# Performance work log

Hardware: AMD Instinct MI355X
Metric: run time of the kernel (lower is better)

Reference implementation:

```python
import jax, jax.numpy as jnp
import numpy as np
import math

B, C, H, W = 32, 256, 56, 56
M = 16            # num_frequency_mixtures
MIX = 4           # sqrt(M)
K = 8             # num_fourier_basis + 1
HID = 16
STRIDE = (1, 1)
EPS = 1e-5


def setup_inputs() -> dict:
    key = jax.random.key(0)
    ks = jax.random.split(key, 8)
    return {
        "x": jax.random.normal(ks[0], (B, C, H, W), jnp.float32),
        "fc1_w": jax.random.normal(ks[1], (HID, C), jnp.float32) * 0.08,
        "fc1_b": jnp.zeros((HID,), jnp.float32),
        "ln_g": jnp.ones((HID,), jnp.float32),
        "ln_b": jnp.zeros((HID,), jnp.float32),
        "fh_w": jax.random.normal(ks[2], (C * M * K, HID), jnp.float32) * 0.08,
        "fh_b": jnp.zeros((C * M * K,), jnp.float32),
        "basis_real": jax.random.normal(ks[3], (K, 56, 32), jnp.float32) * 0.5,
        "basis_imag": jax.random.normal(ks[4], (K, 56, 32), jnp.float32) * 0.5,
        "conv_w": jax.random.normal(ks[5], (C, C), jnp.float32) * (1.0 / math.sqrt(C)),
        "bn_g": jnp.ones((C,), jnp.float32),
        "bn_b": jnp.zeros((C,), jnp.float32),
    }


def reference(x, fc1_w, fc1_b, ln_g, ln_b, fh_w, fh_b,
              basis_real, basis_imag, conv_w, bn_g, bn_b):
    b, c, h, w = x.shape
    # --- FrequencyAttention: GAP -> fc1 -> LN -> ReLU -> fourier_head ---
    ctx = x.mean(axis=(2, 3))                          # (B, C)
    hdn = ctx @ fc1_w.T + fc1_b                        # (B, HID)
    mu = hdn.mean(-1, keepdims=True)
    var = hdn.var(-1, keepdims=True)
    hdn = (hdn - mu) / jnp.sqrt(var + EPS) * ln_g + ln_b
    hdn = jax.nn.relu(hdn)
    att = hdn @ fh_w.T + fh_b                          # (B, C*M*K)

    coeffs = jax.nn.softmax(att.reshape(b, c, M, K), axis=-1)  # (B,C,M,K)

    # --- work-canvas sizes ---
    h_out, w_out = h // STRIDE[0], w // STRIDE[1]
    h_work = math.ceil(h / MIX) * MIX                  # 56
    w_f = w // 2 + 1                                   # 29
    w_f_work = math.ceil(w_f / MIX) * MIX              # 32
    w_work = (w_f_work - 1) * 2 if w_f_work > 1 else 1 # 62

    if (h_work, w_work) != (h, w):
        x_work = jax.image.resize(x, (b, c, h_work, w_work), "bilinear")
    else:
        x_work = x

    x_ft = jnp.fft.rfft2(x_work, s=(h_work, w_work), norm="ortho")  # (B,C,Hw,Wfw) complex
    wf = x_ft.shape[-1]                                # == w_f_work
    ph, pwf = h_work // MIX, wf // MIX                 # 14, 8

    basis = jax.lax.complex(basis_real, basis_imag)    # (K, Hw, Wfw)
    basis_p = basis.reshape(K, MIX, ph, MIX, pwf).transpose(1, 3, 0, 2, 4)
    basis_p = basis_p.reshape(M, K, ph, pwf)           # (M,K,ph,pwf)

    x_ft_p = x_ft.reshape(b, c, MIX, ph, MIX, pwf).transpose(0, 2, 4, 1, 3, 5)
    x_ft_p = x_ft_p.reshape(b, M, c, ph, pwf)          # (B,M,C,ph,pwf)

    coeffs_c = jax.lax.complex(coeffs, jnp.zeros_like(coeffs))
    coeffs_p = coeffs_c.transpose(0, 2, 1, 3)          # (B,M,C,K)

    kernel = jnp.einsum("bmck,mkhw->bmchw", coeffs_p, basis_p)  # (B,M,C,ph,pwf)
    out_ft_p = x_ft_p * kernel

    out_ft = out_ft_p.reshape(b, MIX, MIX, c, ph, pwf).transpose(0, 3, 1, 4, 2, 5)
    out_ft = out_ft.reshape(b, c, h_work, wf)

    s_work = (h_work // STRIDE[0], w_work // STRIDE[1])
    y = jnp.fft.irfft2(out_ft, s=s_work, norm="ortho")  # (B,C,56,62)

    if y.shape[2:] != (h_out, w_out):
        y = jax.image.resize(y, (b, c, h_out, w_out), "bilinear")

    # --- 1x1 conv + BatchNorm (batch statistics, training-mode math) ---
    y = jnp.einsum("bchw,oc->bohw", y, conv_w)
    m = y.mean(axis=(0, 2, 3))
    v = y.var(axis=(0, 2, 3))
    y = (y - m[None, :, None, None]) / jnp.sqrt(v + EPS)[None, :, None, None]
    y = y * bn_g[None, :, None, None] + bn_b[None, :, None, None]
    return y
```

## Files before the change

kernel.cpp:

```cpp
#include <hip/hip_runtime.h>
#include <math.h>

typedef __attribute__((ext_vector_type(4))) float f32x4;
typedef __attribute__((ext_vector_type(8))) short s16x8;
typedef __attribute__((ext_vector_type(4))) short s16x4;
typedef unsigned short ushort_t;

#define MFMA16(a, b, c) __builtin_amdgcn_mfma_f32_16x16x32_bf16((a), (b), (c), 0, 0, 0)

#define WO_CTX    0u
#define WO_HDN    32768u
#define WO_BNSUM  34816u
#define WO_BNSQ   35840u
#define WO_SCALE  36864u
#define WO_SHIFT  37888u
#define WO_COEF   40960u
#define WO_BMT_H  4235264u
#define WO_BMT_L  4243456u
#define WO_FARE_H 4251648u
#define WO_FARE_L 4268032u
#define WO_FAIM_H 4284416u
#define WO_FAIM_L 4300800u
#define WO_FDRE_H 4317184u
#define WO_FDRE_L 4333568u
#define WO_FDIM_H 4349952u
#define WO_FDIM_L 4366336u
#define WO_DTT_H  4382720u
#define WO_DTT_L  4390912u
#define WO_CW_H   4399104u
#define WO_CW_L   4530176u
#define WO_YBF    4661248u

__device__ __forceinline__ ushort_t f2bf(float f) {
  unsigned int u = __builtin_bit_cast(unsigned int, f);
  unsigned int r = (u + 0x7fffu + ((u >> 16) & 1u)) >> 16;
  return (ushort_t)r;
}
__device__ __forceinline__ float bf2f(ushort_t h) {
  unsigned int u = ((unsigned int)h) << 16;
  return __builtin_bit_cast(float, u);
}

__device__ double bmat_val(int w, int vv) {
  const int v = vv & 31;
  const bool isI = vv >= 32;
  double accR = 0.0, accI = 0.0;
  for (int wp = 0; wp < 62; ++wp) {
    const double src = (wp + 0.5) * (56.0 / 62.0) - 0.5;
    const int w0 = (int)floor(src);
    const double f = src - (double)w0;
    const double s0 = (w0 >= 0 && w0 <= 55) ? (1.0 - f) : 0.0;
    const double s1 = (w0 + 1 >= 0 && w0 + 1 <= 55) ? f : 0.0;
    const double ssum = s0 + s1;
    double wgt = 0.0;
    if (w == w0) wgt = s0 / ssum;
    else if (w == w0 + 1) wgt = s1 / ssum;
    if (wgt != 0.0) {
      const int p = (v * wp) % 62;
      const double ang = 6.283185307179586476925286766559 * (double)p / 62.0;
      accR += wgt * cos(ang);
      accI -= wgt * sin(ang);
    }
  }
  const double nrm = 1.0 / sqrt(3472.0);
  return (isI ? accI : accR) * nrm;
}

__device__ double dt_val(int kk, int wq) {
  const int v = (kk < 32) ? kk : kk - 32;
  const bool isI = kk >= 32;
  const double ks = 62.0 / 56.0;
  const double src = (wq + 0.5) * ks - 0.5;
  double wsum = 0.0;
  for (int wp = 0; wp < 62; ++wp) {
    const double xx = fabs(src - (double)wp) / ks;
    if (xx < 1.0) wsum += 1.0 - xx;
  }
  const double cv = (v == 0 || v == 31) ? 1.0 : 2.0;
  double accR = 0.0, accI = 0.0;
  for (int wp = 0; wp < 62; ++wp) {
    const double xx = fabs(src - (double)wp) / ks;
    if (xx >= 1.0) continue;
    const double wgt = (1.0 - xx) / wsum;
    double cc, ss;
    if (v == 0)       { cc = 1.0; ss = 0.0; }
    else if (v == 31) { cc = (wp & 1) ? -1.0 : 1.0; ss = 0.0; }
    else {
      const int p = (v * wp) % 62;
      const double ang = 6.283185307179586476925286766559 * (double)p / 62.0;
      cc = cos(ang); ss = sin(ang);
    }
    accR += wgt * cv * cc;
    accI -= wgt * cv * ss;
  }
  const double nrm = 1.0 / sqrt(3472.0);
  return (isI ? -accI : accR) * nrm;
}

__device__ double dt_val_fixed(int kk, int wq) {
  const int v = (kk < 32) ? kk : kk - 32;
  const bool isI = kk >= 32;
  const double ks = 62.0 / 56.0;
  const double src = (wq + 0.5) * ks - 0.5;
  double wsum = 0.0;
  for (int wp = 0; wp < 62; ++wp) {
    const double xx = fabs(src - (double)wp) / ks;
    if (xx < 1.0) wsum += 1.0 - xx;
  }
  const double cv = (v == 0 || v == 31) ? 1.0 : 2.0;
  double accR = 0.0, accI = 0.0;
  for (int wp = 0; wp < 62; ++wp) {
    const double xx = fabs(src - (double)wp) / ks;
    if (xx >= 1.0) continue;
    const double wgt = (1.0 - xx) / wsum;
    double cc, ss;
    if (v == 0)       { cc = 1.0; ss = 0.0; }
    else if (v == 31) { cc = (wp & 1) ? -1.0 : 1.0; ss = 0.0; }
    else {
      const int p = (v * wp) % 62;
      const double ang = 6.283185307179586476925286766559 * (double)p / 62.0;
      cc = cos(ang); ss = sin(ang);
    }
    accR += wgt * cv * cc;
    accI -= wgt * cv * ss;
  }
  const double nrm = 1.0 / sqrt(3472.0);
  return (isI ? accI : accR) * nrm;
}

__device__ __forceinline__ void emit_hilo(ushort_t* hp, ushort_t* lp, int off, double val) {
  const float fv = (float)val;
  const ushort_t h = f2bf(fv);
  const float hf = bf2f(h);
  const ushort_t l = f2bf((float)(val - (double)hf));
  hp[off] = h;
  lp[off] = l;
}

__global__ void k_const(const float* __restrict__ conv_w,
                        ushort_t* BmT_h, ushort_t* BmT_l,
                        ushort_t* FARe_h, ushort_t* FARe_l,
                        ushort_t* FAIm_h, ushort_t* FAIm_l,
                        ushort_t* FDRe_h, ushort_t* FDRe_l,
                        ushort_t* FDIm_h, ushort_t* FDIm_l,
                        ushort_t* DtT_h, ushort_t* DtT_l,
                        ushort_t* W_h, ushort_t* W_l) {
  const int idx = blockIdx.x * 256 + threadIdx.x;
  if (idx < 4096) {
    const int vv = idx >> 6, k = idx & 63;
    const double v = (k < 56) ? bmat_val(k, vv) : 0.0;
    emit_hilo(BmT_h, BmT_l, idx, v);
  } else if (idx < 36864) {
    const int t = (idx - 4096) & 8191;
    const int which = (idx - 4096) >> 13;
    const int row = t >> 7, k = t & 127;
    double val = 0.0;
    if (row < 56 && k < 112) {
      const int h = (k < 56) ? k : k - 56;
      const double ang = 6.283185307179586476925286766559 *
                         (double)((row * h) % 56) / 56.0;
      const double c = cos(ang), s = sin(ang);
      const bool lowk = (k < 56);
      if (which == 0)      val = lowk ? c : s;
      else if (which == 1) val = lowk ? -s : c;
      else if (which == 2) val = lowk ? c : -s;
      else                 val = lowk ? s : c;
    }
    ushort_t* hp = (which == 0) ? FARe_h : (which == 1) ? FAIm_h : (which == 2) ? FDRe_h : FDIm_h;
    ushort_t* lp = (which == 0) ? FARe_l : (which == 1) ? FAIm_l : (which == 2) ? FDRe_l : FDIm_l;
    emit_hilo(hp, lp, t, val);
  } else if (idx < 40960) {
    const int t = idx - 36864;
    const int w = t >> 6, kk = t & 63;
    const double v = (w < 56) ? dt_val_fixed(kk, w) : 0.0;
    emit_hilo(DtT_h, DtT_l, t, v);
  } else if (idx < 106496) {
    const int t = idx - 40960;
    emit_hilo(W_h, W_l, t, (double)conv_w[t]);
  }
}

__global__ __launch_bounds__(256) void k_gap(const float* __restrict__ x,
                                             float* __restrict__ ctx) {
  const int img = blockIdx.x;
  const int tid = threadIdx.x;
  const float4* p4 = (const float4*)(x + (size_t)img * 3136);
  float s = 0.f;
  for (int i = tid; i < 784; i += 256) {
    const float4 v = p4[i];
    s += v.x + v.y + v.z + v.w;
  }
  for (int off = 32; off > 0; off >>= 1) s += __shfl_down(s, off, 64);
  __shared__ float ls[4];
  if ((tid & 63) == 0) ls[tid >> 6] = s;
  __syncthreads();
  if (tid == 0) ctx[img] = (ls[0] + ls[1] + ls[2] + ls[3]) * (1.0f / 3136.0f);
}

__global__ void k_mlp(const float* __restrict__ ctx, const float* __restrict__ fc1_w,
                      const float* __restrict__ fc1_b, const float* __restrict__ ln_g,
                      const float* __restrict__ ln_b, float* __restrict__ hdn) {
  const int b = blockIdx.x;
  const int j = threadIdx.x;
  __shared__ float h[16];
  if (j < 16) {
    const float* cr = ctx + b * 256;
    const float* wr = fc1_w + j * 256;
    float acc = fc1_b[j];
    for (int c0 = 0; c0 < 256; ++c0) acc = fmaf(cr[c0], wr[c0], acc);
    h[j] = acc;
  }
  __syncthreads();
  if (j < 16) {
    float mu = 0.f, m2 = 0.f;
    for (int t = 0; t < 16; ++t) { mu += h[t]; m2 += h[t] * h[t]; }
    mu *= 0.0625f; m2 *= 0.0625f;
    const float var = m2 - mu * mu;
    const float val = (h[j] - mu) / sqrtf(var + 1e-5f) * ln_g[j] + ln_b[j];
    hdn[b * 16 + j] = fmaxf(val, 0.f);
  }
}

__global__ __launch_bounds__(256) void k_coeffs(const float* __restrict__ hdn,
                                                const float* __restrict__ fh_w,
                                                const float* __restrict__ fh_b,
                                                float* __restrict__ coeffs) {
  const int gid = blockIdx.x * 256 + threadIdx.x;
  const int b = gid >> 12;
  const int cm = gid & 4095;
  float hv[16];
  const float* hp = hdn + b * 16;
#pragma unroll
  for (int j = 0; j < 16; ++j) hv[j] = hp[j];
  const int row0 = cm * 8;
  float a[8];
  float mx = -1e30f;
#pragma unroll
  for (int k = 0; k < 8; ++k) {
    const float* wr = fh_w + (size_t)(row0 + k) * 16;
    float acc = fh_b[row0 + k];
#pragma unroll
    for (int j = 0; j < 16; ++j) acc = fmaf(hv[j], wr[j], acc);
    a[k] = acc;
    mx = fmaxf(mx, acc);
  }
  float s = 0.f;
#pragma unroll
  for (int k = 0; k < 8; ++k) { a[k] = expf(a[k] - mx); s += a[k]; }
  const float inv = 1.f / s;
  float* outp = coeffs + (size_t)gid * 8;
#pragma unroll
  for (int k = 0; k < 8; ++k) outp[k] = a[k] * inv;
}

__global__ __launch_bounds__(256) void k_fft(
    const float* __restrict__ x, const float* __restrict__ coeffs,
    const float* __restrict__ basR, const float* __restrict__ basI,
    const ushort_t* __restrict__ BmT_h, const ushort_t* __restrict__ BmT_l,
    const ushort_t* __restrict__ FARe_h, const ushort_t* __restrict__ FARe_l,
    const ushort_t* __restrict__ FAIm_h, const ushort_t* __restrict__ FAIm_l,
    const ushort_t* __restrict__ FDRe_h, const ushort_t* __restrict__ FDRe_l,
    const ushort_t* __restrict__ FDIm_h, const ushort_t* __restrict__ FDIm_l,
    const ushort_t* __restrict__ DtT_h, const ushort_t* __restrict__ DtT_l,
    ushort_t* __restrict__ ybf) {
  __shared__ __align__(16) ushort_t xa[64 * 72];
  __shared__ __align__(16) ushort_t x1T[32 * 136];
  __shared__ __align__(16) ushort_t x2T[32 * 136];
  __shared__ __align__(16) ushort_t ta[64 * 72];
  __shared__ float gf[3584];
  const int img = blockIdx.x;
  const int tid = threadIdx.x;
  const int wave = tid >> 6, lane = tid & 63, col = lane & 15, quad = lane >> 4;
  const f32x4 zf = {0.f, 0.f, 0.f, 0.f};

  {
    unsigned int* za = (unsigned int*)xa;
    unsigned int* z1 = (unsigned int*)x1T;
    unsigned int* z2 = (unsigned int*)x2T;
    for (int i = tid; i < 2304; i += 256) za[i] = 0u;
    for (int i = tid; i < 2176; i += 256) { z1[i] = 0u; z2[i] = 0u; }
  }
  __syncthreads();

  {
    const float4* xp = (const float4*)(x + (size_t)img * 3136);
    for (int f = tid; f < 784; f += 256) {
      const float4 v = xp[f];
      const int h = f / 14, w4 = (f % 14) * 4;
      s16x4 p;
      p[0] = (short)f2bf(v.x); p[1] = (short)f2bf(v.y);
      p[2] = (short)f2bf(v.z); p[3] = (short)f2bf(v.w);
      *(s16x4*)&xa[h * 72 + w4] = p;
    }
    const float* co = coeffs + (size_t)img * 128;
    for (int q = tid; q < 1792; q += 256) {
      const int u = q >> 5, v = q & 31;
      const int m = (u / 14) * 4 + (v >> 3);
      const float* cm = co + m * 8;
      float gr = 0.f, gi = 0.f;
#pragma unroll
      for (int k = 0; k < 8; ++k) {
        gr = fmaf(cm[k], basR[k * 1792 + q], gr);
        gi = fmaf(cm[k], basI[k * 1792 + q], gi);
      }
      gf[q] = gr;
      gf[1792 + q] = gi;
    }
  }
  __syncthreads();

  {
    const int mt = wave;
    const int arow = (mt * 16 + col) * 72;
    const s16x8 a0 = *(const s16x8*)&xa[arow + quad * 8];
    const s16x8 a1 = *(const s16x8*)&xa[arow + 32 + quad * 8];
    const int h0 = mt * 16 + quad * 4;
    for (int nt = 0; nt < 4; ++nt) {
      const int nrow = nt * 16 + col;
      const s16x8 bh0 = *(const s16x8*)&BmT_h[nrow * 64 + quad * 8];
      const s16x8 bl0 = *(const s16x8*)&BmT_l[nrow * 64 + quad * 8];
      const s16x8 bh1 = *(const s16x8*)&BmT_h[nrow * 64 + 32 + quad * 8];
      const s16x8 bl1 = *(const s16x8*)&BmT_l[nrow * 64 + 32 + quad * 8];
      f32x4 acc = zf;
      acc = MFMA16(a0, bh0, acc);
      acc = MFMA16(a0, bl0, acc);
      acc = MFMA16(a1, bh1, acc);
      acc = MFMA16(a1, bl1, acc);
      if (h0 < 56) {
        s16x4 p;
        p[0] = (short)f2bf(acc[0]); p[1] = (short)f2bf(acc[1]);
        p[2] = (short)f2bf(acc[2]); p[3] = (short)f2bf(acc[3]);
        const int vr = nrow & 31;
        const int kk = (nrow < 32) ? h0 : 56 + h0;
        *(s16x4*)&x1T[vr * 136 + kk] = p;
      }
    }
  }
  __syncthreads();

  {
    const int mt = wave;
    f32x4 accRe[2] = {zf, zf}, accIm[2] = {zf, zf};
    for (int ks = 0; ks < 4; ++ks) {
      const int aoff = (mt * 16 + col) * 128 + ks * 32 + quad * 8;
      const s16x8 aRh = *(const s16x8*)&FARe_h[aoff];
      const s16x8 aRl = *(const s16x8*)&FARe_l[aoff];
      const s16x8 aIh = *(const s16x8*)&FAIm_h[aoff];
      const s16x8 aIl = *(const s16x8*)&FAIm_l[aoff];
#pragma unroll
      for (int nt = 0; nt < 2; ++nt) {
        const s16x8 b = *(const s16x8*)&x1T[(nt * 16 + col) * 136 + ks * 32 + quad * 8];
        accRe[nt] = MFMA16(aRh, b, accRe[nt]);
        accRe[nt] = MFMA16(aRl, b, accRe[nt]);
        accIm[nt] = MFMA16(aIh, b, accIm[nt]);
        accIm[nt] = MFMA16(aIl, b, accIm[nt]);
      }
    }
    const int u0 = mt * 16 + quad * 4;
    if (u0 < 56) {
#pragma unroll
      for (int nt = 0; nt < 2; ++nt) {
        const int v = nt * 16 + col;
        s16x4 pR, pI;
#pragma unroll
        for (int r = 0; r < 4; ++r) {
          const int u = u0 + r;
          const float gr = gf[u * 32 + v];
          const float gi = gf[1792 + u * 32 + v];
          const float re = accRe[nt][r] * gr - accIm[nt][r] * gi;
          const float im = accRe[nt][r] * gi + accIm[nt][r] * gr;
          pR[r] = (short)f2bf(re);
          pI[r] = (short)f2bf(im);
        }
        *(s16x4*)&x2T[v * 136 + u0] = pR;
        *(s16x4*)&x2T[v * 136 + 56 + u0] = pI;
      }
    }
  }
  __syncthreads();

  {
    const int mt = wave;
    f32x4 accRe[2] = {zf, zf}, accIm[2] = {zf, zf};
    for (int ks = 0; ks < 4; ++ks) {
      const int aoff = (mt * 16 + col) * 128 + ks * 32 + quad * 8;
      const s16x8 aRh = *(const s16x8*)&FDRe_h[aoff];
      const s16x8 aRl = *(const s16x8*)&FDRe_l[aoff];
      const s16x8 aIh = *(const s16x8*)&FDIm_h[aoff];
      const s16x8 aIl = *(const s16x8*)&FDIm_l[aoff];
#pragma unroll
      for (int nt = 0; nt < 2; ++nt) {
        const s16x8 b = *(const s16x8*)&x2T[(nt * 16 + col) * 136 + ks * 32 + quad * 8];
        accRe[nt] = MFMA16(aRh, b, accRe[nt]);
        accRe[nt] = MFMA16(aRl, b, accRe[nt]);
        accIm[nt] = MFMA16(aIh, b, accIm[nt]);
        accIm[nt] = MFMA16(aIl, b, accIm[nt]);
      }
    }
    const int h0 = mt * 16 + quad * 4;
#pragma unroll
    for (int nt = 0; nt < 2; ++nt) {
      const int v = nt * 16 + col;
#pragma unroll
      for (int r = 0; r < 4; ++r) {
        ta[(h0 + r) * 72 + v]      = f2bf(accRe[nt][r]);
        ta[(h0 + r) * 72 + 32 + v] = f2bf(accIm[nt][r]);
      }
    }
  }
  __syncthreads();

  {
    const int mt = wave;
    const int arow = (mt * 16 + col) * 72;
    const s16x8 a0 = *(const s16x8*)&ta[arow + quad * 8];
    const s16x8 a1 = *(const s16x8*)&ta[arow + 32 + quad * 8];
    const int h0 = mt * 16 + quad * 4;
    ushort_t* yo = ybf + (size_t)img * 3136;
    for (int nt = 0; nt < 4; ++nt) {
      const int w = nt * 16 + col;
      const s16x8 bh0 = *(const s16x8*)&DtT_h[w * 64 + quad * 8];
      const s16x8 bl0 = *(const s16x8*)&DtT_l[w * 64 + quad * 8];
      const s16x8 bh1 = *(const s16x8*)&DtT_h[w * 64 + 32 + quad * 8];
      const s16x8 bl1 = *(const s16x8*)&DtT_l[w * 64 + 32 + quad * 8];
      f32x4 acc = zf;
      acc = MFMA16(a0, bh0, acc);
      acc = MFMA16(a0, bl0, acc);
      acc = MFMA16(a1, bh1, acc);
      acc = MFMA16(a1, bl1, acc);
      if (h0 < 56 && w < 56) {
#pragma unroll
        for (int r = 0; r < 4; ++r) yo[(h0 + r) * 56 + w] = f2bf(acc[r]);
      }
    }
  }
}

__global__ __launch_bounds__(256) void k_conv(const ushort_t* __restrict__ ybf,
                                              const ushort_t* __restrict__ W_h,
                                              const ushort_t* __restrict__ W_l,
                                              float* __restrict__ z) {
  const int pb = blockIdx.x;
  const int oh = blockIdx.y;
  const int b = blockIdx.z;
  const int tid = threadIdx.x;
  const int wave = tid >> 6, lane = tid & 63, col = lane & 15, quad = lane >> 4;
  const f32x4 zf = {0.f, 0.f, 0.f, 0.f};
  f32x4 acc[8][4];
#pragma unroll
  for (int mt = 0; mt < 8; ++mt)
#pragma unroll
    for (int i = 0; i < 4; ++i) acc[mt][i] = zf;

  const size_t ybase = (size_t)b * 256 * 3136;
  int p0i[4];
  bool act[4];
#pragma unroll
  for (int i = 0; i < 4; ++i) {
    p0i[i] = pb * 256 + (wave * 4 + i) * 16;
    act[i] = p0i[i] < 3136;
  }

  for (int ks = 0; ks < 8; ++ks) {
    const int c0 = ks * 32 + quad * 8;
    s16x8 bfr[4];
#pragma unroll
    for (int i = 0; i < 4; ++i) {
      if (act[i]) {
        s16x8 t;
#pragma unroll
        for (int j = 0; j < 8; ++j)
          t[j] = (short)ybf[ybase + (size_t)(c0 + j) * 3136 + p0i[i] + col];
        bfr[i] = t;
      }
    }
#pragma unroll
    for (int mt = 0; mt < 8; ++mt) {
      const int orow = oh * 128 + mt * 16 + col;
      const s16x8 ah = *(const s16x8*)&W_h[orow * 256 + ks * 32 + quad * 8];
      const s16x8 al = *(const s16x8*)&W_l[orow * 256 + ks * 32 + quad * 8];
#pragma unroll
      for (int i = 0; i < 4; ++i) {
        if (act[i]) {
          acc[mt][i] = MFMA16(ah, bfr[i], acc[mt][i]);
          acc[mt][i] = MFMA16(al, bfr[i], acc[mt][i]);
        }
      }
    }
  }

#pragma unroll
  for (int mt = 0; mt < 8; ++mt) {
#pragma unroll
    for (int i = 0; i < 4; ++i) {
      if (!act[i]) continue;
#pragma unroll
      for (int r = 0; r < 4; ++r) {
        const int o = oh * 128 + mt * 16 + quad * 4 + r;
        z[((size_t)b * 256 + o) * 3136 + p0i[i] + col] = acc[mt][i][r];
      }
    }
  }
}

__global__ __launch_bounds__(256) void k_bnsum(const float* __restrict__ z,
                                               float* __restrict__ bnsum,
                                               float* __restrict__ bnsq) {
  const int bo = blockIdx.x;
  const int tid = threadIdx.x;
  const float4* p4 = (const float4*)(z + (size_t)bo * 3136);
  float s = 0.f, s2 = 0.f;
  for (int i = tid; i < 784; i += 256) {
    const float4 v = p4[i];
    s += v.x + v.y + v.z + v.w;
    s2 += v.x * v.x + v.y * v.y + v.z * v.z + v.w * v.w;
  }
  for (int off = 32; off > 0; off >>= 1) {
    s += __shfl_down(s, off, 64);
    s2 += __shfl_down(s2, off, 64);
  }
  __shared__ float ls[8];
  if ((tid & 63) == 0) { ls[tid >> 6] = s; ls[4 + (tid >> 6)] = s2; }
  __syncthreads();
  if (tid == 0) {
    atomicAdd(bnsum + (bo & 255), ls[0] + ls[1] + ls[2] + ls[3]);
    atomicAdd(bnsq + (bo & 255), ls[4] + ls[5] + ls[6] + ls[7]);
  }
}

__global__ void k_bnstats(const float* __restrict__ bnsum, const float* __restrict__ bnsq,
                          const float* __restrict__ bn_g, const float* __restrict__ bn_b,
                          float* __restrict__ scale, float* __restrict__ shift) {
  const int o = threadIdx.x;
  if (o < 256) {
    const float N = 32.f * 3136.f;
    const float m = bnsum[o] / N;
    const float v = bnsq[o] / N - m * m;
    const float sc = bn_g[o] / sqrtf(v + 1e-5f);
    scale[o] = sc;
    shift[o] = bn_b[o] - m * sc;
  }
}

__global__ __launch_bounds__(256) void k_bnapply(float* __restrict__ z,
                                                 const float* __restrict__ scale,
                                                 const float* __restrict__ shift) {
  const size_t i = ((size_t)blockIdx.x * 256 + threadIdx.x) * 4;
  const int ch = (int)((i / 3136) & 255);
  const float sc = scale[ch], sh = shift[ch];
  float4 v = *(float4*)(z + i);
  v.x = fmaf(v.x, sc, sh);
  v.y = fmaf(v.y, sc, sh);
  v.z = fmaf(v.z, sc, sh);
  v.w = fmaf(v.w, sc, sh);
  *(float4*)(z + i) = v;
}

extern "C" void kernel_launch(void* const* d_in, const int* in_sizes, int n_in,
                              void* d_out, int out_size, void* d_ws, size_t ws_size,
                              hipStream_t stream) {
  const float* x          = (const float*)d_in[0];
  const float* fc1_w      = (const float*)d_in[1];
  const float* fc1_b      = (const float*)d_in[2];
  const float* ln_g       = (const float*)d_in[3];
  const float* ln_b       = (const float*)d_in[4];
  const float* fh_w       = (const float*)d_in[5];
  const float* fh_b       = (const float*)d_in[6];
  const float* basis_real = (const float*)d_in[7];
  const float* basis_imag = (const float*)d_in[8];
  const float* conv_w     = (const float*)d_in[9];
  const float* bn_g       = (const float*)d_in[10];
  const float* bn_b       = (const float*)d_in[11];
  float* out = (float*)d_out;
  char* ws = (char*)d_ws;
  (void)in_sizes; (void)n_in; (void)out_size; (void)ws_size;

  float* ctx   = (float*)(ws + WO_CTX);
  float* hdn   = (float*)(ws + WO_HDN);
  float* bnsum = (float*)(ws + WO_BNSUM);
  float* bnsq  = (float*)(ws + WO_BNSQ);
  float* scale = (float*)(ws + WO_SCALE);
  float* shift = (float*)(ws + WO_SHIFT);
  float* coef  = (float*)(ws + WO_COEF);
  ushort_t* BmT_h  = (ushort_t*)(ws + WO_BMT_H);
  ushort_t* BmT_l  = (ushort_t*)(ws + WO_BMT_L);
  ushort_t* FARe_h = (ushort_t*)(ws + WO_FARE_H);
  ushort_t* FARe_l = (ushort_t*)(ws + WO_FARE_L);
  ushort_t* FAIm_h = (ushort_t*)(ws + WO_FAIM_H);
  ushort_t* FAIm_l = (ushort_t*)(ws + WO_FAIM_L);
  ushort_t* FDRe_h = (ushort_t*)(ws + WO_FDRE_H);
  ushort_t* FDRe_l = (ushort_t*)(ws + WO_FDRE_L);
  ushort_t* FDIm_h = (ushort_t*)(ws + WO_FDIM_H);
  ushort_t* FDIm_l = (ushort_t*)(ws + WO_FDIM_L);
  ushort_t* DtT_h  = (ushort_t*)(ws + WO_DTT_H);
  ushort_t* DtT_l  = (ushort_t*)(ws + WO_DTT_L);
  ushort_t* W_h    = (ushort_t*)(ws + WO_CW_H);
  ushort_t* W_l    = (ushort_t*)(ws + WO_CW_L);
  ushort_t* ybf    = (ushort_t*)(ws + WO_YBF);

  hipMemsetAsync(bnsum, 0, 2048, stream);

  hipLaunchKernelGGL(k_const, dim3(416), dim3(256), 0, stream,
                     conv_w, BmT_h, BmT_l, FARe_h, FARe_l, FAIm_h, FAIm_l,
                     FDRe_h, FDRe_l, FDIm_h, FDIm_l, DtT_h, DtT_l, W_h, W_l);
  hipLaunchKernelGGL(k_gap, dim3(8192), dim3(256), 0, stream, x, ctx);
  hipLaunchKernelGGL(k_mlp, dim3(32), dim3(64), 0, stream,
                     ctx, fc1_w, fc1_b, ln_g, ln_b, hdn);
  hipLaunchKernelGGL(k_coeffs, dim3(512), dim3(256), 0, stream, hdn, fh_w, fh_b, coef);
  hipLaunchKernelGGL(k_fft, dim3(8192), dim3(256), 0, stream,
                     x, coef, basis_real, basis_imag,
                     BmT_h, BmT_l, FARe_h, FARe_l, FAIm_h, FAIm_l,
                     FDRe_h, FDRe_l, FDIm_h, FDIm_l, DtT_h, DtT_l, ybf);
  hipLaunchKernelGGL(k_conv, dim3(13, 2, 32), dim3(256), 0, stream, ybf, W_h, W_l, out);
  hipLaunchKernelGGL(k_bnsum, dim3(8192), dim3(256), 0, stream, out, bnsum, bnsq);
  hipLaunchKernelGGL(k_bnstats, dim3(1), dim3(256), 0, stream,
                     bnsum, bnsq, bn_g, bn_b, scale, shift);
  hipLaunchKernelGGL(k_bnapply, dim3(25088), dim3(256), 0, stream, out, scale, shift);
}
```

Measured before the change: 713.0 us.

## Restructure FFT kernel to one image per wave and fuse BN sums into conv

The FFT kernel now has each wave own one whole image in its own shared-memory slice, with four images per block. This removes the block-wide barriers between FFT stages. The spectral kernel G is built once per block from a pre-interleaved basis stored as packed bf16, and x is loaded straight from global memory into MFMA fragments. The conv kernel stages its activations through shared memory so the loads coalesce, and it accumulates the BatchNorm sums with shuffle reductions and atomics, which removes the separate k_bnsum pass over the output. The trade-offs are more per-wave work and register pressure, and G is now held in lower precision.

```diff
diff --git a/kernel.cpp b/kernel.cpp
--- a/kernel.cpp
+++ b/kernel.cpp
@@ -29,7 +29,8 @@
 #define WO_DTT_L  4390912u
 #define WO_CW_H   4399104u
 #define WO_CW_L   4530176u
-#define WO_YBF    4661248u
+#define WO_BASP   4661248u
+#define WO_YBF    4775936u
 
 __device__ __forceinline__ ushort_t f2bf(float f) {
   unsigned int u = __builtin_bit_cast(unsigned int, f);
@@ -39,6 +40,14 @@
 __device__ __forceinline__ float bf2f(ushort_t h) {
   unsigned int u = ((unsigned int)h) << 16;
   return __builtin_bit_cast(float, u);
+}
+__device__ __forceinline__ s16x8 pack8(float4 a, float4 b) {
+  s16x8 r;
+  r[0] = (short)f2bf(a.x); r[1] = (short)f2bf(a.y);
+  r[2] = (short)f2bf(a.z); r[3] = (short)f2bf(a.w);
+  r[4] = (short)f2bf(b.x); r[5] = (short)f2bf(b.y);
+  r[6] = (short)f2bf(b.z); r[7] = (short)f2bf(b.w);
+  return r;
 }
 
 __device__ double bmat_val(int w, int vv) {
@@ -66,7 +75,7 @@
   return (isI ? accI : accR) * nrm;
 }
 
-__device__ double dt_val(int kk, int wq) {
+__device__ double dt_val_fixed(int kk, int wq) {
   const int v = (kk < 32) ? kk : kk - 32;
   const bool isI = kk >= 32;
   const double ks = 62.0 / 56.0;
@@ -94,37 +103,6 @@
     accI -= wgt * cv * ss;
   }
   const double nrm = 1.0 / sqrt(3472.0);
-  return (isI ? -accI : accR) * nrm;
-}
-
-__device__ double dt_val_fixed(int kk, int wq) {
-  const int v = (kk < 32) ? kk : kk - 32;
-  const bool isI = kk >= 32;
-  const double ks = 62.0 / 56.0;
-  const double src = (wq + 0.5) * ks - 0.5;
-  double wsum = 0.0;
-  for (int wp = 0; wp < 62; ++wp) {
-    const double xx = fabs(src - (double)wp) / ks;
-    if (xx < 1.0) wsum += 1.0 - xx;
-  }
-  const double cv = (v == 0 || v == 31) ? 1.0 : 2.0;
-  double accR = 0.0, accI = 0.0;
-  for (int wp = 0; wp < 62; ++wp) {
-    const double xx = fabs(src - (double)wp) / ks;
-    if (xx >= 1.0) continue;
-    const double wgt = (1.0 - xx) / wsum;
-    double cc, ss;
-    if (v == 0)       { cc = 1.0; ss = 0.0; }
-    else if (v == 31) { cc = (wp & 1) ? -1.0 : 1.0; ss = 0.0; }
-    else {
-      const int p = (v * wp) % 62;
-      const double ang = 6.283185307179586476925286766559 * (double)p / 62.0;
-      cc = cos(ang); ss = sin(ang);
-    }
-    accR += wgt * cv * cc;
-    accI -= wgt * cv * ss;
-  }
-  const double nrm = 1.0 / sqrt(3472.0);
   return (isI ? accI : accR) * nrm;
 }
 
@@ -138,13 +116,15 @@
 }
 
 __global__ void k_const(const float* __restrict__ conv_w,
+                        const float* __restrict__ basR, const float* __restrict__ basI,
                         ushort_t* BmT_h, ushort_t* BmT_l,
                         ushort_t* FARe_h, ushort_t* FARe_l,
                         ushort_t* FAIm_h, ushort_t* FAIm_l,
                         ushort_t* FDRe_h, ushort_t* FDRe_l,
                         ushort_t* FDIm_h, ushort_t* FDIm_l,
                         ushort_t* DtT_h, ushort_t* DtT_l,
-                        ushort_t* W_h, ushort_t* W_l) {
+                        ushort_t* W_h, ushort_t* W_l,
+                        float* basP) {
   const int idx = blockIdx.x * 256 + threadIdx.x;
   if (idx < 4096) {
     const int vv = idx >> 6, k = idx & 63;
@@ -177,6 +157,10 @@
   } else if (idx < 106496) {
     const int t = idx - 40960;
     emit_hilo(W_h, W_l, t, (double)conv_w[t]);
+  } else if (idx < 135168) {
+    const int t = idx - 106496;
+    const int q = t >> 4, r = t & 15, k = r >> 1;
+    basP[t] = (r & 1) ? basI[k * 1792 + q] : basR[k * 1792 + q];
   }
 }
 
@@ -255,7 +239,7 @@
 
 __global__ __launch_bounds__(256) void k_fft(
     const float* __restrict__ x, const float* __restrict__ coeffs,
-    const float* __restrict__ basR, const float* __restrict__ basI,
+    const float* __restrict__ basP,
     const ushort_t* __restrict__ BmT_h, const ushort_t* __restrict__ BmT_l,
     const ushort_t* __restrict__ FARe_h, const ushort_t* __restrict__ FARe_l,
     const ushort_t* __restrict__ FAIm_h, const ushort_t* __restrict__ FAIm_l,
@@ -263,174 +247,208 @@
     const ushort_t* __restrict__ FDIm_h, const ushort_t* __restrict__ FDIm_l,
     const ushort_t* __restrict__ DtT_h, const ushort_t* __restrict__ DtT_l,
     ushort_t* __restrict__ ybf) {
-  __shared__ __align__(16) ushort_t xa[64 * 72];
-  __shared__ __align__(16) ushort_t x1T[32 * 136];
-  __shared__ __align__(16) ushort_t x2T[32 * 136];
-  __shared__ __align__(16) ushort_t ta[64 * 72];
-  __shared__ float gf[3584];
-  const int img = blockIdx.x;
+  __shared__ __align__(16) ushort_t buf[4 * 4600];
+  __shared__ unsigned int Gsh[4 * 1792];
+  const int img0 = blockIdx.x * 4;
   const int tid = threadIdx.x;
   const int wave = tid >> 6, lane = tid & 63, col = lane & 15, quad = lane >> 4;
   const f32x4 zf = {0.f, 0.f, 0.f, 0.f};
+  ushort_t* bufw = buf + wave * 4600;
+  const int img = img0 + wave;
 
   {
-    unsigned int* za = (unsigned int*)xa;
-    unsigned int* z1 = (unsigned int*)x1T;
-    unsigned int* z2 = (unsigned int*)x2T;
-    for (int i = tid; i < 2304; i += 256) za[i] = 0u;
-    for (int i = tid; i < 2176; i += 256) { z1[i] = 0u; z2[i] = 0u; }
+    const int row = lane >> 1, half = lane & 1;
+    s16x8 z8;
+#pragma unroll
+    for (int j = 0; j < 8; ++j) z8[j] = 0;
+    *(s16x8*)&bufw[row * 136 + 112 + half * 8] = z8;
+  }
+
+  for (int it = 0; it < 8; ++it) {
+    if (tid < 224) {
+      const int m = it * 2 + (tid >= 112 ? 1 : 0);
+      const int idx = (tid >= 112) ? tid - 112 : tid;
+      const int u = (m >> 2) * 14 + (idx >> 3);
+      const int v = (m & 3) * 8 + (idx & 7);
+      const int q = u * 32 + v;
+      const float4* bp = (const float4*)(basP + q * 16);
+      const float4 b0 = bp[0], b1 = bp[1], b2 = bp[2], b3 = bp[3];
+#pragma unroll
+      for (int i = 0; i < 4; ++i) {
+        const float* cm = coeffs + ((size_t)(img0 + i) * 16 + m) * 8;
+        float gr = 0.f, gi = 0.f;
+        gr = fmaf(cm[0], b0.x, gr); gi = fmaf(cm[0], b0.y, gi);
+        gr = fmaf(cm[1], b0.z, gr); gi = fmaf(cm[1], b0.w, gi);
+        gr = fmaf(cm[2], b1.x, gr); gi = fmaf(cm[2], b1.y, gi);
+        gr = fmaf(cm[3], b1.z, gr); gi = fmaf(cm[3], b1.w, gi);
+        gr = fmaf(cm[4], b2.x, gr); gi = fmaf(cm[4], b2.y, gi);
+        gr = fmaf(cm[5], b2.z, gr); gi = fmaf(cm[5], b2.w, gi);
+        gr = fmaf(cm[6], b3.x, gr); gi = fmaf(cm[6], b3.y, gi);
+        gr = fmaf(cm[7], b3.z, gr); gi = fmaf(cm[7], b3.w, gi);
+        Gsh[i * 1792 + q] = (((unsigned int)f2bf(gr)) << 16) | (unsigned int)f2bf(gi);
+      }
+    }
   }
   __syncthreads();
 
   {
-    const float4* xp = (const float4*)(x + (size_t)img * 3136);
-    for (int f = tid; f < 784; f += 256) {
-      const float4 v = xp[f];
-      const int h = f / 14, w4 = (f % 14) * 4;
-      s16x4 p;
-      p[0] = (short)f2bf(v.x); p[1] = (short)f2bf(v.y);
-      p[2] = (short)f2bf(v.z); p[3] = (short)f2bf(v.w);
-      *(s16x4*)&xa[h * 72 + w4] = p;
-    }
-    const float* co = coeffs + (size_t)img * 128;
-    for (int q = tid; q < 1792; q += 256) {
-      const int u = q >> 5, v = q & 31;
-      const int m = (u / 14) * 4 + (v >> 3);
-      const float* cm = co + m * 8;
-      float gr = 0.f, gi = 0.f;
-#pragma unroll
-      for (int k = 0; k < 8; ++k) {
-        gr = fmaf(cm[k], basR[k * 1792 + q], gr);
-        gi = fmaf(cm[k], basI[k * 1792 + q], gi);
-      }
-      gf[q] = gr;
-      gf[1792 + q] = gi;
-    }
-  }
-  __syncthreads();
+    const float* xim = x + (size_t)img * 3136;
+#pragma unroll
+    for (int mt = 0; mt < 4; ++mt) {
+      const int h = mt * 16 + col;
+      const int hc = (h < 56) ? h : 55;
+      const float* xr = xim + hc * 56;
+      const float4 xa0 = *(const float4*)(xr + quad * 8);
+      const float4 xa1 = *(const float4*)(xr + quad * 8 + 4);
+      const s16x8 a0 = pack8(xa0, xa1);
+      s16x8 a1;
+      if (quad < 3) {
+        const float4 xb0 = *(const float4*)(xr + 32 + quad * 8);
+        const float4 xb1 = *(const float4*)(xr + 36 + quad * 8);
+        a1 = pack8(xb0, xb1);
+      } else {
+#pragma unroll
+        for (int j = 0; j < 8; ++j) a1[j] = 0;
+      }
+      const int h0 = mt * 16 + quad * 4;
+#pragma unroll
+      for (int nt = 0; nt < 4; ++nt) {
+        const int nrow = nt * 16 + col;
+        const s16x8 bh0 = *(const s16x8*)&BmT_h[nrow * 64 + quad * 8];
+        const s16x8 bl0 = *(const s16x8*)&BmT_l[nrow * 64 + quad * 8];
+        const s16x8 bh1 = *(const s16x8*)&BmT_h[nrow * 64 + 32 + quad * 8];
+        const s16x8 bl1 = *(const s16x8*)&BmT_l[nrow * 64 + 32 + quad * 8];
+        f32x4 acc = zf;
+        acc = MFMA16(a0, bh0, acc);
+        acc = MFMA16(a0, bl0, acc);
+        acc = MFMA16(a1, bh1, acc);
+        acc = MFMA16(a1, bl1, acc);
+        if (h0 < 56) {
+          s16x4 p;
+          p[0] = (short)f2bf(acc[0]); p[1] = (short)f2bf(acc[1]);
+          p[2] = (short)f2bf(acc[2]); p[3] = (short)f2bf(acc[3]);
+          const int vr = nrow & 31;
+          const int kk = (nrow < 32) ? h0 : 56 + h0;
+          *(s16x4*)&bufw[vr * 136 + kk] = p;
+        }
+      }
+    }
+  }
 
   {
-    const int mt = wave;
-    const int arow = (mt * 16 + col) * 72;
-    const s16x8 a0 = *(const s16x8*)&xa[arow + quad * 8];
-    const s16x8 a1 = *(const s16x8*)&xa[arow + 32 + quad * 8];
-    const int h0 = mt * 16 + quad * 4;
-    for (int nt = 0; nt < 4; ++nt) {
-      const int nrow = nt * 16 + col;
-      const s16x8 bh0 = *(const s16x8*)&BmT_h[nrow * 64 + quad * 8];
-      const s16x8 bl0 = *(const s16x8*)&BmT_l[nrow * 64 + quad * 8];
-      const s16x8 bh1 = *(const s16x8*)&BmT_h[nrow * 64 + 32 + quad * 8];
-      const s16x8 bl1 = *(const s16x8*)&BmT_l[nrow * 64 + 32 + quad * 8];
-      f32x4 acc = zf;
-      acc = MFMA16(a0, bh0, acc);
-      acc = MFMA16(a0, bl0, acc);
-      acc = MFMA16(a1, bh1, acc);
-      acc = MFMA16(a1, bl1, acc);
+    s16x8 bf[2][4];
+#pragma unroll
+    for (int nt = 0; nt < 2; ++nt)
+#pragma unroll
+      for (int ks = 0; ks < 4; ++ks)
+        bf[nt][ks] = *(const s16x8*)&bufw[(nt * 16 + col) * 136 + ks * 32 + quad * 8];
+
+#pragma unroll
+    for (int mt = 0; mt < 4; ++mt) {
+      f32x4 aR[2] = {zf, zf}, aI[2] = {zf, zf};
+#pragma unroll
+      for (int ks = 0; ks < 4; ++ks) {
+        const int off = (mt * 16 + col) * 128 + ks * 32 + quad * 8;
+        const s16x8 rh = *(const s16x8*)&FARe_h[off];
+        const s16x8 rl = *(const s16x8*)&FARe_l[off];
+        const s16x8 ih = *(const s16x8*)&FAIm_h[off];
+        const s16x8 il = *(const s16x8*)&FAIm_l[off];
+#pragma unroll
+        for (int nt = 0; nt < 2; ++nt) {
+          aR[nt] = MFMA16(rh, bf[nt][ks], aR[nt]);
+          aR[nt] = MFMA16(rl, bf[nt][ks], aR[nt]);
+          aI[nt] = MFMA16(ih, bf[nt][ks], aI[nt]);
+          aI[nt] = MFMA16(il, bf[nt][ks], aI[nt]);
+        }
+      }
+      const int u0 = mt * 16 + quad * 4;
+      if (u0 < 56) {
+#pragma unroll
+        for (int nt = 0; nt < 2; ++nt) {
+          const int v = nt * 16 + col;
+          s16x4 pR, pI;
+#pragma unroll
+          for (int r = 0; r < 4; ++r) {
+            const unsigned int gp = Gsh[wave * 1792 + (u0 + r) * 32 + v];
+            const float gr = __builtin_bit_cast(float, gp & 0xffff0000u);
+            const float gi = __builtin_bit_cast(float, gp << 16);
+            const float re = aR[nt][r] * gr - aI[nt][r] * gi;
+            const float im = aR[nt][r] * gi + aI[nt][r] * gr;
+            pR[r] = (short)f2bf(re);
+            pI[r] = (short)f2bf(im);
+          }
+          *(s16x4*)&bufw[v * 136 + u0] = pR;
+          *(s16x4*)&bufw[v * 136 + 56 + u0] = pI;
+        }
+      }
+    }
+  }
+
+  {
+    s16x8 bf[2][4];
+#pragma unroll
+    for (int nt = 0; nt < 2; ++nt)
+#pragma unroll
+      for (int ks = 0; ks < 4; ++ks)
+        bf[nt][ks] = *(const s16x8*)&bufw[(nt * 16 + col) * 136 + ks * 32 + quad * 8];
+
+#pragma unroll
+    for (int mt = 0; mt < 4; ++mt) {
+      f32x4 aR[2] = {zf, zf}, aI[2] = {zf, zf};
+#pragma unroll
+      for (int ks = 0; ks < 4; ++ks) {
+        const int off = (mt * 16 + col) * 128 + ks * 32 + quad * 8;
+        const s16x8 rh = *(const s16x8*)&FDRe_h[off];
+        const s16x8 rl = *(const s16x8*)&FDRe_l[off];
+        const s16x8 ih = *(const s16x8*)&FDIm_h[off];
+        const s16x8 il = *(const s16x8*)&FDIm_l[off];
+#pragma unroll
+        for (int nt = 0; nt < 2; ++nt) {
+          aR[nt] = MFMA16(rh, bf[nt][ks], aR[nt]);
+          aR[nt] = MFMA16(rl, bf[nt][ks], aR[nt]);
+          aI[nt] = MFMA16(ih, bf[nt][ks], aI[nt]);
+          aI[nt] = MFMA16(il, bf[nt][ks], aI[nt]);
+        }
+      }
+      const int h0 = mt * 16 + quad * 4;
       if (h0 < 56) {
-        s16x4 p;
-        p[0] = (short)f2bf(acc[0]); p[1] = (short)f2bf(acc[1]);
-        p[2] = (short)f2bf(acc[2]); p[3] = (short)f2bf(acc[3]);
-        const int vr = nrow & 31;
-        const int kk = (nrow < 32) ? h0 : 56 + h0;
-        *(s16x4*)&x1T[vr * 136 + kk] = p;
-      }
-    }
-  }
-  __syncthreads();
+#pragma unroll
+        for (int nt = 0; nt < 2; ++nt) {
+          const int v = nt * 16 + col;
+#pragma unroll
+          for (int r = 0; r < 4; ++r) {
+            bufw[(h0 + r) * 72 + v]      = f2bf(aR[nt][r]);
+            bufw[(h0 + r) * 72 + 32 + v] = f2bf(aI[nt][r]);
+          }
+        }
+      }
+    }
+  }
 
   {
-    const int mt = wave;
-    f32x4 accRe[2] = {zf, zf}, accIm[2] = {zf, zf};
-    for (int ks = 0; ks < 4; ++ks) {
-      const int aoff = (mt * 16 + col) * 128 + ks * 32 + quad * 8;
-      const s16x8 aRh = *(const s16x8*)&FARe_h[aoff];
-      const s16x8 aRl = *(const s16x8*)&FARe_l[aoff];
-      const s16x8 aIh = *(const s16x8*)&FAIm_h[aoff];
-      const s16x8 aIl = *(const s16x8*)&FAIm_l[aoff];
-#pragma unroll
-      for (int nt = 0; nt < 2; ++nt) {
-        const s16x8 b = *(const s16x8*)&x1T[(nt * 16 + col) * 136 + ks * 32 + quad * 8];
-        accRe[nt] = MFMA16(aRh, b, accRe[nt]);
-        accRe[nt] = MFMA16(aRl, b, accRe[nt]);
-        accIm[nt] = MFMA16(aIh, b, accIm[nt]);
-        accIm[nt] = MFMA16(aIl, b, accIm[nt]);
-      }
-    }
-    const int u0 = mt * 16 + quad * 4;
-    if (u0 < 56) {
-#pragma unroll
-      for (int nt = 0; nt < 2; ++nt) {
-        const int v = nt * 16 + col;
-        s16x4 pR, pI;
-#pragma unroll
-        for (int r = 0; r < 4; ++r) {
-          const int u = u0 + r;
-          const float gr = gf[u * 32 + v];
-          const float gi = gf[1792 + u * 32 + v];
-          const float re = accRe[nt][r] * gr - accIm[nt][r] * gi;
-          const float im = accRe[nt][r] * gi + accIm[nt][r] * gr;
-          pR[r] = (short)f2bf(re);
-          pI[r] = (short)f2bf(im);
+    ushort_t* yo = ybf + (size_t)img * 3136;
+#pragma unroll
+    for (int mt = 0; mt < 4; ++mt) {
+      const int arow = (mt * 16 + col) * 72;
+      const s16x8 a0 = *(const s16x8*)&bufw[arow + quad * 8];
+      const s16x8 a1 = *(const s16x8*)&bufw[arow + 32 + quad * 8];
+      const int h0 = mt * 16 + quad * 4;
+#pragma unroll
+      for (int nt = 0; nt < 4; ++nt) {
+        const int w = nt * 16 + col;
+        const s16x8 bh0 = *(const s16x8*)&DtT_h[w * 64 + quad * 8];
+        const s16x8 bl0 = *(const s16x8*)&DtT_l[w * 64 + quad * 8];
+        const s16x8 bh1 = *(const s16x8*)&DtT_h[w * 64 + 32 + quad * 8];
+        const s16x8 bl1 = *(const s16x8*)&DtT_l[w * 64 + 32 + quad * 8];
+        f32x4 acc = zf;
+        acc = MFMA16(a0, bh0, acc);
+        acc = MFMA16(a0, bl0, acc);
+        acc = MFMA16(a1, bh1, acc);
+        acc = MFMA16(a1, bl1, acc);
+        if (h0 < 56 && w < 56) {
+#pragma unroll
+          for (int r = 0; r < 4; ++r) yo[(h0 + r) * 56 + w] = f2bf(acc[r]);
         }
-        *(s16x4*)&x2T[v * 136 + u0] = pR;
-        *(s16x4*)&x2T[v * 136 + 56 + u0] = pI;
-      }
-    }
-  }
-  __syncthreads();
-
-  {
-    const int mt = wave;
-    f32x4 accRe[2] = {zf, zf}, accIm[2] = {zf, zf};
-    for (int ks = 0; ks < 4; ++ks) {
-      const int aoff = (mt * 16 + col) * 128 + ks * 32 + quad * 8;
-      const s16x8 aRh = *(const s16x8*)&FDRe_h[aoff];
-      const s16x8 aRl = *(const s16x8*)&FDRe_l[aoff];
-      const s16x8 aIh = *(const s16x8*)&FDIm_h[aoff];
-      const s16x8 aIl = *(const s16x8*)&FDIm_l[aoff];
-#pragma unroll
-      for (int nt = 0; nt < 2; ++nt) {
-        const s16x8 b = *(const s16x8*)&x2T[(nt * 16 + col) * 136 + ks * 32 + quad * 8];
-        accRe[nt] = MFMA16(aRh, b, accRe[nt]);
-        accRe[nt] = MFMA16(aRl, b, accRe[nt]);
-        accIm[nt] = MFMA16(aIh, b, accIm[nt]);
-        accIm[nt] = MFMA16(aIl, b, accIm[nt]);
-      }
-    }
-    const int h0 = mt * 16 + quad * 4;
-#pragma unroll
-    for (int nt = 0; nt < 2; ++nt) {
-      const int v = nt * 16 + col;
-#pragma unroll
-      for (int r = 0; r < 4; ++r) {
-        ta[(h0 + r) * 72 + v]      = f2bf(accRe[nt][r]);
-        ta[(h0 + r) * 72 + 32 + v] = f2bf(accIm[nt][r]);
-      }
-    }
-  }
-  __syncthreads();
-
-  {
-    const int mt = wave;
-    const int arow = (mt * 16 + col) * 72;
-    const s16x8 a0 = *(const s16x8*)&ta[arow + quad * 8];
-    const s16x8 a1 = *(const s16x8*)&ta[arow + 32 + quad * 8];
-    const int h0 = mt * 16 + quad * 4;
-    ushort_t* yo = ybf + (size_t)img * 3136;
-    for (int nt = 0; nt < 4; ++nt) {
-      const int w = nt * 16 + col;
-      const s16x8 bh0 = *(const s16x8*)&DtT_h[w * 64 + quad * 8];
-      const s16x8 bl0 = *(const s16x8*)&DtT_l[w * 64 + quad * 8];
-      const s16x8 bh1 = *(const s16x8*)&DtT_h[w * 64 + 32 + quad * 8];
-      const s16x8 bl1 = *(const s16x8*)&DtT_l[w * 64 + 32 + quad * 8];
-      f32x4 acc = zf;
-      acc = MFMA16(a0, bh0, acc);
-      acc = MFMA16(a0, bl0, acc);
-      acc = MFMA16(a1, bh1, acc);
-      acc = MFMA16(a1, bl1, acc);
-      if (h0 < 56 && w < 56) {
-#pragma unroll
-        for (int r = 0; r < 4; ++r) yo[(h0 + r) * 56 + w] = f2bf(acc[r]);
       }
     }
   }
@@ -439,10 +457,13 @@
 __global__ __launch_bounds__(256) void k_conv(const ushort_t* __restrict__ ybf,
                                               const ushort_t* __restrict__ W_h,
                                               const ushort_t* __restrict__ W_l,
-                                              float* __restrict__ z) {
+                                              float* __restrict__ z,
+                                              float* __restrict__ bnsum,
+                                              float* __restrict__ bnsq) {
+  __shared__ __align__(16) ushort_t Ys[256 * 40];
   const int pb = blockIdx.x;
   const int oh = blockIdx.y;
-  const int b = blockIdx.z;
+  const int b  = blockIdx.z;
   const int tid = threadIdx.x;
   const int wave = tid >> 6, lane = tid & 63, col = lane & 15, quad = lane >> 4;
   const f32x4 zf = {0.f, 0.f, 0.f, 0.f};
@@ -453,26 +474,37 @@
     for (int i = 0; i < 4; ++i) acc[mt][i] = zf;
 
   const size_t ybase = (size_t)b * 256 * 3136;
-  int p0i[4];
-  bool act[4];
-#pragma unroll
-  for (int i = 0; i < 4; ++i) {
-    p0i[i] = pb * 256 + (wave * 4 + i) * 16;
-    act[i] = p0i[i] < 3136;
-  }
+  const int pbase = pb * 256;
+  const int chl = tid >> 3;
+  const int pg  = tid & 7;
 
   for (int ks = 0; ks < 8; ++ks) {
-    const int c0 = ks * 32 + quad * 8;
-    s16x8 bfr[4];
+    const int c = ks * 32 + chl;
+    s16x8 ld[4];
+#pragma unroll
+    for (int j = 0; j < 4; ++j) {
+      const int p = pbase + pg * 32 + j * 8;
+      if (p < 3136) {
+        ld[j] = *(const s16x8*)&ybf[ybase + (size_t)c * 3136 + p];
+      } else {
+#pragma unroll
+        for (int e = 0; e < 8; ++e) ld[j][e] = 0;
+      }
+    }
+    __syncthreads();
+#pragma unroll
+    for (int j = 0; j < 4; ++j) {
+      const int pl = pg * 32 + j * 8;
+#pragma unroll
+      for (int e = 0; e < 8; ++e) Ys[(pl + e) * 40 + chl] = (ushort_t)ld[j][e];
+    }
+    __syncthreads();
+
+    s16x8 bfrag[4];
 #pragma unroll
     for (int i = 0; i < 4; ++i) {
-      if (act[i]) {
-        s16x8 t;
-#pragma unroll
-        for (int j = 0; j < 8; ++j)
-          t[j] = (short)ybf[ybase + (size_t)(c0 + j) * 3136 + p0i[i] + col];
-        bfr[i] = t;
-      }
+      const int pl = wave * 64 + i * 16 + col;
+      bfrag[i] = *(const s16x8*)&Ys[pl * 40 + quad * 8];
     }
 #pragma unroll
     for (int mt = 0; mt < 8; ++mt) {
@@ -481,50 +513,45 @@
       const s16x8 al = *(const s16x8*)&W_l[orow * 256 + ks * 32 + quad * 8];
 #pragma unroll
       for (int i = 0; i < 4; ++i) {
-        if (act[i]) {
-          acc[mt][i] = MFMA16(ah, bfr[i], acc[mt][i]);
-          acc[mt][i] = MFMA16(al, bfr[i], acc[mt][i]);
+        acc[mt][i] = MFMA16(ah, bfrag[i], acc[mt][i]);
+        acc[mt][i] = MFMA16(al, bfrag[i], acc[mt][i]);
+      }
+    }
+  }
+
+#pragma unroll
+  for (int mt = 0; mt < 8; ++mt) {
+    float s[4] = {0.f, 0.f, 0.f, 0.f}, s2[4] = {0.f, 0.f, 0.f, 0.f};
+#pragma unroll
+    for (int i = 0; i < 4; ++i) {
+      const int p = pbase + wave * 64 + i * 16 + col;
+      if (p < 3136) {
+#pragma unroll
+        for (int r = 0; r < 4; ++r) {
+          const int o = oh * 128 + mt * 16 + quad * 4 + r;
+          const float v = acc[mt][i][r];
+          z[((size_t)b * 256 + o) * 3136 + p] = v;
+          s[r] += v;
+          s2[r] += v * v;
         }
       }
     }
-  }
-
-#pragma unroll
-  for (int mt = 0; mt < 8; ++mt) {
-#pragma unroll
-    for (int i = 0; i < 4; ++i) {
-      if (!act[i]) continue;
+#pragma unroll
+    for (int mask = 1; mask < 16; mask <<= 1) {
+#pragma unroll
+      for (int r = 0; r < 4; ++r) {
+        s[r] += __shfl_xor(s[r], mask, 64);
+        s2[r] += __shfl_xor(s2[r], mask, 64);
+      }
+    }
+    if (col == 0) {
 #pragma unroll
       for (int r = 0; r < 4; ++r) {
         const int o = oh * 128 + mt * 16 + quad * 4 + r;
-        z[((size_t)b * 256 + o) * 3136 + p0i[i] + col] = acc[mt][i][r];
-      }
-    }
-  }
-}
-
-__global__ __launch_bounds__(256) void k_bnsum(const float* __restrict__ z,
-                                               float* __restrict__ bnsum,
-                                               float* __restrict__ bnsq) {
-  const int bo = blockIdx.x;
-  const int tid = threadIdx.x;
-  const float4* p4 = (const float4*)(z + (size_t)bo * 3136);
-  float s = 0.f, s2 = 0.f;
-  for (int i = tid; i < 784; i += 256) {
-    const float4 v = p4[i];
-    s += v.x + v.y + v.z + v.w;
-    s2 += v.x * v.x + v.y * v.y + v.z * v.z + v.w * v.w;
-  }
-  for (int off = 32; off > 0; off >>= 1) {
-    s += __shfl_down(s, off, 64);
-    s2 += __shfl_down(s2, off, 64);
-  }
-  __shared__ float ls[8];
-  if ((tid & 63) == 0) { ls[tid >> 6] = s; ls[4 + (tid >> 6)] = s2; }
-  __syncthreads();
-  if (tid == 0) {
-    atomicAdd(bnsum + (bo & 255), ls[0] + ls[1] + ls[2] + ls[3]);
-    atomicAdd(bnsq + (bo & 255), ls[4] + ls[5] + ls[6] + ls[7]);
+        atomicAdd(bnsum + o, s[r]);
+        atomicAdd(bnsq + o, s2[r]);
+      }
+    }
   }
 }
 
@@ -596,23 +623,25 @@
   ushort_t* DtT_l  = (ushort_t*)(ws + WO_DTT_L);
   ushort_t* W_h    = (ushort_t*)(ws + WO_CW_H);
   ushort_t* W_l    = (ushort_t*)(ws + WO_CW_L);
+  float*    basP   = (float*)(ws + WO_BASP);
   ushort_t* ybf    = (ushort_t*)(ws + WO_YBF);
 
   hipMemsetAsync(bnsum, 0, 2048, stream);
 
-  hipLaunchKernelGGL(k_const, dim3(416), dim3(256), 0, stream,
-                     conv_w, BmT_h, BmT_l, FARe_h, FARe_l, FAIm_h, FAIm_l,
-                     FDRe_h, FDRe_l, FDIm_h, FDIm_l, DtT_h, DtT_l, W_h, W_l);
+  hipLaunchKernelGGL(k_const, dim3(528), dim3(256), 0, stream,
+                     conv_w, basis_real, basis_imag,
+                     BmT_h, BmT_l, FARe_h, FARe_l, FAIm_h, FAIm_l,
+                     FDRe_h, FDRe_l, FDIm_h, FDIm_l, DtT_h, DtT_l, W_h, W_l, basP);
   hipLaunchKernelGGL(k_gap, dim3(8192), dim3(256), 0, stream, x, ctx);
   hipLaunchKernelGGL(k_mlp, dim3(32), dim3(64), 0, stream,
                      ctx, fc1_w, fc1_b, ln_g, ln_b, hdn);
   hipLaunchKernelGGL(k_coeffs, dim3(512), dim3(256), 0, stream, hdn, fh_w, fh_b, coef);
-  hipLaunchKernelGGL(k_fft, dim3(8192), dim3(256), 0, stream,
-                     x, coef, basis_real, basis_imag,
+  hipLaunchKernelGGL(k_fft, dim3(2048), dim3(256), 0, stream,
+                     x, coef, basP,
                      BmT_h, BmT_l, FARe_h, FARe_l, FAIm_h, FAIm_l,
                      FDRe_h, FDRe_l, FDIm_h, FDIm_l, DtT_h, DtT_l, ybf);
-  hipLaunchKernelGGL(k_conv, dim3(13, 2, 32), dim3(256), 0, stream, ybf, W_h, W_l, out);
-  hipLaunchKernelGGL(k_bnsum, dim3(8192), dim3(256), 0, stream, out, bnsum, bnsq);
+  hipLaunchKernelGGL(k_conv, dim3(13, 2, 32), dim3(256), 0, stream,
+                     ybf, W_h, W_l, out, bnsum, bnsq);
   hipLaunchKernelGGL(k_bnstats, dim3(1), dim3(256), 0, stream,
                      bnsum, bnsq, bn_g, bn_b, scale, shift);
   hipLaunchKernelGGL(k_bnapply, dim3(25088), dim3(256), 0, stream, out, scale, shift);
```

Result: slower. 766.0 us (+7.4%).
